# Optimization experiments

Hardware: AMD Instinct MI355X
Metric: run time of the kernel (lower is better)

Reference implementation:

```python
import math
import jax, jax.numpy as jnp
import numpy as np

NUM_HEADS, RAD_PTS, LVL_PTS = 8, 4, 1
P = RAD_PTS * LVL_PTS


def setup_inputs() -> dict:
    B, Nq, Din = 2, 21760, 256
    hw = np.array([[128, 128], [64, 64], [32, 32], [16, 16]], np.int64)
    sizes = hw[:, 0] * hw[:, 1]
    offs = np.concatenate([[0], np.cumsum(sizes)[:-1]]).astype(np.int64)
    Ns = int(sizes.sum())
    map_ids = np.tile(np.repeat(np.arange(4), sizes)[None], (B, 1)).astype(np.int64)

    key = jax.random.key(0)
    ks = jax.random.split(key, 8)
    in_feats = jax.random.normal(ks[0], (B, Nq, Din), jnp.float32)
    sample_feats = jax.random.normal(ks[1], (B, Ns, Din), jnp.float32)
    sample_priors = jax.random.uniform(ks[2], (B, Nq, 2), jnp.float32)

    # sample_offsets bias: radial grid init as in the torch module
    thetas = np.arange(NUM_HEADS) * (2.0 * math.pi / NUM_HEADS)
    grid = np.stack([np.cos(thetas), np.sin(thetas), np.zeros(NUM_HEADS)], 1)
    grid = grid / np.abs(grid).max(1, keepdims=True)
    grid = np.tile(grid.reshape(NUM_HEADS, 1, 1, 3), (1, RAD_PTS, LVL_PTS, 1))
    grid = grid * np.arange(1, RAD_PTS + 1).reshape(1, RAD_PTS, 1, 1)
    bo = jnp.asarray(grid.reshape(-1), jnp.float32)

    Wo = jax.random.normal(ks[3], (NUM_HEADS * P * 3, Din), jnp.float32) * 0.01
    Wa = jax.random.normal(ks[4], (NUM_HEADS * P, Din), jnp.float32) * 0.01
    ba = jnp.zeros((NUM_HEADS * P,), jnp.float32)
    s = 1.0 / np.sqrt(Din)
    Wv = jax.random.normal(ks[5], (Din, Din), jnp.float32) * s
    bv = jnp.zeros((Din,), jnp.float32)
    Wout = jax.random.normal(ks[6], (Din, Din), jnp.float32) * s
    bout = jnp.zeros((Din,), jnp.float32)

    return dict(in_feats=in_feats, sample_priors=sample_priors, sample_feats=sample_feats,
                map_hw=jnp.asarray(hw), map_offs=jnp.asarray(offs), map_ids=jnp.asarray(map_ids),
                Wo=Wo, bo=bo, Wa=Wa, ba=ba, Wv=Wv, bv=bv, Wout=Wout, bout=bout)


def _trilinear_sample(val, map_hw, map_offs, xy, z, L):
    # val [B,Ns,H,D]; xy [B,Q,H,P,2] normalized; z [B,Q,H,P] in ~[0,1]
    B, Ns, H, D = val.shape
    Q = xy.shape[1]
    val_t = val.transpose(0, 2, 1, 3)  # [B,H,Ns,D]
    x, y = xy[..., 0], xy[..., 1]
    lvl_f = z * (L - 1)
    l0 = jnp.floor(lvl_f).astype(jnp.int32)
    wz = lvl_f - l0.astype(lvl_f.dtype)

    def gather(idx):  # idx [B,Q,H,P] int32 -> [B,Q,H,P,D]
        it = idx.transpose(0, 2, 1, 3).reshape(B, H, Q * P, 1)
        g = jnp.take_along_axis(val_t, it, axis=2)  # [B,H,Q*P,D]
        return g.reshape(B, H, Q, P, D).transpose(0, 2, 1, 3, 4)

    def sample_level(lvl):  # bilinear sample within pyramid level `lvl` (zero padding)
        valid_l = (lvl >= 0) & (lvl < L)
        lc = jnp.clip(lvl, 0, L - 1)
        Hl = map_hw[lc, 0].astype(jnp.int32)
        Wl = map_hw[lc, 1].astype(jnp.int32)
        off = map_offs[lc].astype(jnp.int32)
        xf = x * Wl.astype(x.dtype) - 0.5
        yf = y * Hl.astype(x.dtype) - 0.5
        x0 = jnp.floor(xf).astype(jnp.int32)
        y0 = jnp.floor(yf).astype(jnp.int32)
        dx = xf - x0.astype(x.dtype)
        dy = yf - y0.astype(x.dtype)
        out = jnp.zeros((B, Q, H, P, D), x.dtype)
        corners = [(x0, y0, (1 - dx) * (1 - dy)), (x0 + 1, y0, dx * (1 - dy)),
                   (x0, y0 + 1, (1 - dx) * dy), (x0 + 1, y0 + 1, dx * dy)]
        for xi, yi, w in corners:
            ok = valid_l & (xi >= 0) & (xi < Wl) & (yi >= 0) & (yi < Hl)
            idx = off + jnp.clip(yi, 0, Hl - 1) * Wl + jnp.clip(xi, 0, Wl - 1)
            out = out + gather(idx) * (w * ok.astype(x.dtype))[..., None]
        return out

    return sample_level(l0) * (1 - wz)[..., None] + sample_level(l0 + 1) * wz[..., None]


def reference(in_feats, sample_priors, sample_feats, map_hw, map_offs, map_ids,
              Wo, bo, Wa, ba, Wv, bv, Wout, bout):
    B, Nq, _ = in_feats.shape
    Ns = sample_feats.shape[1]
    L = map_hw.shape[0]
    D = Wv.shape[0] // NUM_HEADS

    val = (sample_feats @ Wv.T + bv).reshape(B, Ns, NUM_HEADS, D)
    offs = (in_feats @ Wo.T + bo).reshape(B, Nq, NUM_HEADS, P, 3)

    # sample_priors last dim == 2: normalize offsets by (W, H) of the query's map
    norm = map_hw[:, ::-1][map_ids].astype(offs.dtype)  # [B,Nq,2] (w,h)
    sample_xy = sample_priors[:, :, None, None, :2] + offs[..., :2] / norm[:, :, None, None, :]

    lvl_off = jnp.arange(LVL_PTS, dtype=offs.dtype) - 0.5 * (LVL_PTS - 1)
    z_grid = map_ids[:, :, None, None, None].astype(offs.dtype) + lvl_off  # [B,Nq,1,1,Lp]
    z_grid = jnp.broadcast_to(z_grid, (B, Nq, NUM_HEADS, RAD_PTS, LVL_PTS)).reshape(B, Nq, NUM_HEADS, P)
    sample_z = (z_grid + jnp.tanh(offs[..., 2])) / (L - 1)

    attn = jax.nn.softmax((in_feats @ Wa.T + ba).reshape(B, Nq, NUM_HEADS, P), axis=3)

    sampled = _trilinear_sample(val, map_hw, map_offs, sample_xy, sample_z, L)  # [B,Nq,H,P,D]
    attn_feats = jnp.einsum('bqhpd,bqhp->bqhd', sampled, attn).reshape(B, Nq, NUM_HEADS * D)
    return attn_feats @ Wout.T + bout
```

## Files before the change

### kernel.cpp

```cpp
#include <hip/hip_runtime.h>
#include <hip/hip_bf16.h>
#include <math.h>

typedef __bf16 bf16x8 __attribute__((ext_vector_type(8)));
typedef float f32x4 __attribute__((ext_vector_type(4)));
typedef float f32x2 __attribute__((ext_vector_type(2)));
typedef unsigned short ushort8 __attribute__((ext_vector_type(8)));

static __device__ __forceinline__ unsigned short f2bf(float f) {
    union { float f; unsigned u; } c; c.f = f;
    unsigned r = c.u + 0x7FFFu + ((c.u >> 16) & 1u);
    return (unsigned short)(r >> 16);
}

static __device__ __forceinline__ void gload_lds16(
    const unsigned short* g, unsigned short* l)
{
    __builtin_amdgcn_global_load_lds(
        (const __attribute__((address_space(1))) void*)g,
        (__attribute__((address_space(3))) void*)l, 16, 0, 0);
}

__global__ __launch_bounds__(256) void convert_weights_hist(
    const float* __restrict__ Wv, const float* __restrict__ Wo,
    const float* __restrict__ Wa, const float* __restrict__ Wout,
    const float* __restrict__ bo, const float* __restrict__ ba,
    unsigned short* __restrict__ Wv_b, unsigned short* __restrict__ Woa_b,
    unsigned short* __restrict__ Wout_b, float* __restrict__ boa,
    const float* __restrict__ priors, int* __restrict__ counts,
    int BQ, int Nq)
{
    __shared__ int cnt[16];
    if (threadIdx.x < 16) cnt[threadIdx.x] = 0;
    __syncthreads();

    int gid = blockIdx.x * blockDim.x + threadIdx.x;
    int stride = gridDim.x * blockDim.x;
    for (int i = gid; i < 163840; i += stride) {
        if (i < 65536)       Wv_b[i] = f2bf(Wv[i]);
        else if (i < 90112)  Woa_b[i - 65536] = f2bf(Wo[i - 65536]);
        else if (i < 98304)  Woa_b[i - 65536] = f2bf(Wa[i - 90112]);
        else                 Wout_b[i - 98304] = f2bf(Wout[i - 98304]);
    }
    if (gid < 96)       boa[gid] = bo[gid];
    else if (gid < 128) boa[gid] = ba[gid - 96];

    for (int q = gid; q < BQ; q += stride) {
        int b = q / Nq;
        float py = priors[(size_t)q * 2 + 1];
        int band = min(7, max(0, (int)(py * 8.0f)));
        atomicAdd(&cnt[b * 8 + band], 1);
    }
    __syncthreads();
    if (threadIdx.x < 16 && cnt[threadIdx.x] > 0)
        atomicAdd(&counts[threadIdx.x], cnt[threadIdx.x]);
}

__global__ __launch_bounds__(256) void bucket_scatter(
    const float* __restrict__ priors, const int* __restrict__ counts,
    int* __restrict__ cursors, int* __restrict__ qidx, int BQ, int Nq)
{
    __shared__ int lcnt[16];
    __shared__ int lbase[16];
    const int tid = threadIdx.x;
    if (tid < 16) lcnt[tid] = 0;
    __syncthreads();
    int q = blockIdx.x * 256 + tid;
    int mybucket = 0, myslot = 0;
    bool valid = q < BQ;
    if (valid) {
        int b = q / Nq;
        float py = priors[(size_t)q * 2 + 1];
        int band = min(7, max(0, (int)(py * 8.0f)));
        mybucket = b * 8 + band;
        myslot = atomicAdd(&lcnt[mybucket], 1);
    }
    __syncthreads();
    if (tid < 16) {
        int base = 0;
        #pragma unroll
        for (int i = 0; i < 16; ++i) base += (i < tid) ? counts[i] : 0;
        lbase[tid] = base + atomicAdd(&cursors[tid], lcnt[tid]);
    }
    __syncthreads();
    if (valid) qidx[lbase[mybucket] + myslot] = q;
}

template<int WN, bool A_BF16, int OUT_MODE>
__global__ __launch_bounds__(WN * 64) void gemm_mfma(
    const void* __restrict__ Av, const unsigned short* __restrict__ W,
    const float* __restrict__ bias, void* __restrict__ Cv,
    int M, int N, int K, int NsPB)
{
    constexpr int BM = 64;
    constexpr int BN = WN * 64;
    constexpr int BK = 64;
    constexpr int NTHR = WN * 64;
    constexpr int LDP = 72;
    constexpr int ASZ = A_BF16 ? (BM * 64) : (BM * LDP);

    __shared__ __align__(16) unsigned short As[ASZ];
    __shared__ __align__(16) unsigned short Bs[BN * 64];

    const int bm  = blockIdx.x * BM;
    const int bn  = blockIdx.y * BN;
    const int tid = threadIdx.x;
    const int wid = tid >> 6;
    const int lane = tid & 63;
    const int lr = lane & 15;
    const int lg = lane >> 4;
    const int lrow = lane >> 3;
    const int lc16 = (lane & 7) ^ (lrow & 7);

    f32x4 acc[4][4];
    #pragma unroll
    for (int mi = 0; mi < 4; ++mi)
        #pragma unroll
        for (int ni = 0; ni < 4; ++ni)
            acc[mi][ni] = (f32x4){0.f, 0.f, 0.f, 0.f};

    for (int kt = 0; kt < K; kt += BK) {
        #pragma unroll
        for (int c = wid; c < BN / 8; c += WN) {
            const unsigned short* g =
                W + (size_t)(bn + c * 8 + lrow) * K + kt + lc16 * 8;
            gload_lds16(g, Bs + c * 512);
        }
        if (A_BF16) {
            const unsigned short* A = (const unsigned short*)Av;
            #pragma unroll
            for (int c = wid; c < BM / 8; c += WN) {
                const unsigned short* g =
                    A + (size_t)(bm + c * 8 + lrow) * K + kt + lc16 * 8;
                gload_lds16(g, As + c * 512);
            }
        } else {
            const float* A = (const float*)Av;
            #pragma unroll
            for (int u = tid; u < BM * 8; u += NTHR) {
                int r = u >> 3, kb = u & 7;
                const float* src = A + (size_t)(bm + r) * K + kt + kb * 8;
                float4 f0 = *(const float4*)(src);
                float4 f1 = *(const float4*)(src + 4);
                ushort8 v;
                v[0] = f2bf(f0.x); v[1] = f2bf(f0.y);
                v[2] = f2bf(f0.z); v[3] = f2bf(f0.w);
                v[4] = f2bf(f1.x); v[5] = f2bf(f1.y);
                v[6] = f2bf(f1.z); v[7] = f2bf(f1.w);
                *(ushort8*)(As + r * LDP + kb * 8) = v;
            }
        }
        __syncthreads();

        #pragma unroll
        for (int kk = 0; kk < 2; ++kk) {
            bf16x8 fa[4], fb[4];
            #pragma unroll
            for (int mi = 0; mi < 4; ++mi) {
                if (A_BF16) {
                    int row = mi * 16 + lr;
                    fa[mi] = *(const bf16x8*)(As + row * 64 +
                                              ((kk * 4 + lg) ^ (lr & 7)) * 8);
                } else {
                    fa[mi] = *(const bf16x8*)(As + (mi * 16 + lr) * LDP +
                                              kk * 32 + lg * 8);
                }
            }
            #pragma unroll
            for (int ni = 0; ni < 4; ++ni) {
                int row = wid * 64 + ni * 16 + lr;
                fb[ni] = *(const bf16x8*)(Bs + row * 64 +
                                          ((kk * 4 + lg) ^ (lr & 7)) * 8);
            }
            #pragma unroll
            for (int mi = 0; mi < 4; ++mi)
                #pragma unroll
                for (int ni = 0; ni < 4; ++ni)
                    acc[mi][ni] = __builtin_amdgcn_mfma_f32_16x16x32_bf16(
                        fa[mi], fb[ni], acc[mi][ni], 0, 0, 0);
        }
        __syncthreads();
    }

    if (OUT_MODE == 2) {
        const int b = bm / NsPB;
        const int ns_base = bm - b * NsPB;
        #pragma unroll
        for (int ni = 0; ni < 4; ++ni) {
            int col = wid * 64 + ni * 16 + lr;
            int h   = col >> 5;
            int ch  = col & 31;
            float bv = bias[col];
            unsigned short* dst = (unsigned short*)Cv +
                (size_t)(b * 8 + h) * NsPB * 32 + ch;
            #pragma unroll
            for (int mi = 0; mi < 4; ++mi) {
                #pragma unroll
                for (int r = 0; r < 4; ++r) {
                    int ns = ns_base + mi * 16 + lg * 4 + r;
                    dst[(size_t)ns * 32] = f2bf(acc[mi][ni][r] + bv);
                }
            }
        }
    } else {
        #pragma unroll
        for (int ni = 0; ni < 4; ++ni) {
            int col = bn + wid * 64 + ni * 16 + lr;
            float bv = bias[col];
            #pragma unroll
            for (int mi = 0; mi < 4; ++mi) {
                #pragma unroll
                for (int r = 0; r < 4; ++r) {
                    int row = bm + mi * 16 + lg * 4 + r;
                    if (OUT_MODE == 1) {
                        ((unsigned short*)Cv)[(size_t)row * N + col] =
                            f2bf(acc[mi][ni][r] + bv);
                    } else {
                        ((float*)Cv)[(size_t)row * N + col] = acc[mi][ni][r] + bv;
                    }
                }
            }
        }
    }
}

__global__ __launch_bounds__(256) void msda_sample_kernel(
    const float* __restrict__ C1,
    const float* __restrict__ priors,
    const unsigned short* __restrict__ val,
    const int*   __restrict__ map_hw,
    const int*   __restrict__ map_offs,
    const int*   __restrict__ map_ids,
    const int*   __restrict__ qidx,
    unsigned short* __restrict__ out,
    int Nq, int Ns)
{
    const int swz = (blockIdx.x & 7) * (gridDim.x >> 3) + (blockIdx.x >> 3);
    const int qh  = threadIdx.x >> 7;
    const int bq  = qidx[swz * 2 + qh];
    const int t   = threadIdx.x & 127;
    const int b   = bq / Nq;
    const int q   = bq - b * Nq;

    __shared__ float s_w[2][32][9];
    __shared__ int   s_i[2][32][9];
    __shared__ float s_red[2][32][9];

    if (t < 64) {
        const int hp = t >> 1;
        const int sl = t & 1;
        const float* sc = C1 + (size_t)bq * 128;
        float o0 = sc[hp * 3 + 0];
        float o1 = sc[hp * 3 + 1];
        float o2 = sc[hp * 3 + 2];
        float logit = sc[96 + hp];

        float m = logit;
        m = fmaxf(m, __shfl_xor(m, 2));
        m = fmaxf(m, __shfl_xor(m, 4));
        float e = expf(logit - m);
        float s = e;
        s += __shfl_xor(s, 2);
        s += __shfl_xor(s, 4);
        float attnw = e / s;

        int lid = map_ids[(size_t)b * Ns + q];
        float px = priors[(size_t)bq * 2 + 0];
        float py = priors[(size_t)bq * 2 + 1];
        int Hq = map_hw[lid * 2 + 0];
        int Wq = map_hw[lid * 2 + 1];
        float x = px + o0 / (float)Wq;
        float y = py + o1 / (float)Hq;

        float lvl_f = (float)lid + tanhf(o2);
        float l0f = floorf(lvl_f);
        int   l0  = (int)l0f;
        float wz  = lvl_f - l0f;

        const int   lv = l0 + sl;
        const float wl = sl ? wz : (1.0f - wz);
        float w4[4];
        int   i4[4];
        if (lv >= 0 && lv < 4) {
            int Hs  = map_hw[lv * 2 + 0];
            int Ws  = map_hw[lv * 2 + 1];
            int off = map_offs[lv];
            float xf = x * (float)Ws - 0.5f;
            float yf = y * (float)Hs - 0.5f;
            float x0f = floorf(xf), y0f = floorf(yf);
            int   x0  = (int)x0f,  y0  = (int)y0f;
            float dx = xf - x0f, dy = yf - y0f;
            #pragma unroll
            for (int j = 0; j < 4; ++j) {
                int xi = x0 + (j & 1);
                int yi = y0 + (j >> 1);
                float w = ((j & 1) ? dx : 1.0f - dx) *
                          ((j >> 1) ? dy : 1.0f - dy);
                bool ok = (xi >= 0) && (xi < Ws) && (yi >= 0) && (yi < Hs);
                w4[j] = ok ? (w * wl * attnw) : 0.0f;
                i4[j] = ok ? ((off + yi * Ws + xi) << 6) : 0;
            }
        } else {
            #pragma unroll
            for (int j = 0; j < 4; ++j) { w4[j] = 0.0f; i4[j] = 0; }
        }
        #pragma unroll
        for (int j = 0; j < 4; ++j) {
            s_w[qh][hp][sl * 4 + j] = w4[j];
            s_i[qh][hp][sl * 4 + j] = i4[j];
        }
    }
    __syncthreads();

    const int p  = t >> 5;
    const int s  = t & 31;
    const int h  = s >> 2;
    const int d8 = s & 3;
    const int hp = h * 4 + p;

    float w[8];
    int   ix[8];
    #pragma unroll
    for (int j = 0; j < 8; ++j) { w[j] = s_w[qh][hp][j]; ix[j] = s_i[qh][hp][j]; }

    const char* vbase = (const char*)(val + (size_t)(b * 8 + h) * Ns * 32) + d8 * 16;
    f32x2 acc2[4];
    #pragma unroll
    for (int k = 0; k < 4; ++k) acc2[k] = (f32x2){0.f, 0.f};

    #pragma unroll
    for (int j = 0; j < 8; ++j) {
        uint4 u = *(const uint4*)(vbase + ix[j]);
        f32x2 w2 = {w[j], w[j]};
        unsigned ua[4] = {u.x, u.y, u.z, u.w};
        #pragma unroll
        for (int k = 0; k < 4; ++k) {
            union { unsigned u; float f; } lo, hi;
            lo.u = ua[k] << 16;
            hi.u = ua[k] & 0xffff0000u;
            f32x2 v2 = {lo.f, hi.f};
            acc2[k] += w2 * v2;
        }
    }

    #pragma unroll
    for (int k = 0; k < 4; ++k) {
        acc2[k][0] += __shfl_xor(acc2[k][0], 32);
        acc2[k][1] += __shfl_xor(acc2[k][1], 32);
    }

    if (t >= 64 && t < 96) {
        #pragma unroll
        for (int k = 0; k < 4; ++k) {
            s_red[qh][t - 64][2 * k]     = acc2[k][0];
            s_red[qh][t - 64][2 * k + 1] = acc2[k][1];
        }
    }
    __syncthreads();

    if (t < 32) {
        ushort8 o;
        #pragma unroll
        for (int k = 0; k < 4; ++k) {
            o[2 * k]     = f2bf(acc2[k][0] + s_red[qh][t][2 * k]);
            o[2 * k + 1] = f2bf(acc2[k][1] + s_red[qh][t][2 * k + 1]);
        }
        *(ushort8*)(out + (size_t)bq * 256 + t * 8) = o;
    }
}

extern "C" void kernel_launch(void* const* d_in, const int* in_sizes, int n_in,
                              void* d_out, int out_size, void* d_ws, size_t ws_size,
                              hipStream_t stream) {
    const float* in_feats      = (const float*)d_in[0];
    const float* sample_priors = (const float*)d_in[1];
    const float* sample_feats  = (const float*)d_in[2];
    const int*   map_hw        = (const int*)d_in[3];
    const int*   map_offs      = (const int*)d_in[4];
    const int*   map_ids       = (const int*)d_in[5];
    const float* Wo            = (const float*)d_in[6];
    const float* bo            = (const float*)d_in[7];
    const float* Wa            = (const float*)d_in[8];
    const float* ba            = (const float*)d_in[9];
    const float* Wv            = (const float*)d_in[10];
    const float* bv            = (const float*)d_in[11];
    const float* Wout          = (const float*)d_in[12];
    const float* bout          = (const float*)d_in[13];
    float* out = (float*)d_out;

    const int B = 2, Nq = 21760, Din = 256;
    const int Ns = in_sizes[2] / (B * Din);
    const int BQ = B * Nq;

    unsigned short* val = (unsigned short*)d_out;
    float* C1 = (float*)d_ws;
    unsigned short* af = (unsigned short*)((char*)d_ws + (size_t)BQ * 128 * 4);
    char* wbase = (char*)d_ws + (size_t)BQ * 128 * 4 + (size_t)BQ * 256 * 2;
    unsigned short* Wv_b   = (unsigned short*)wbase;
    unsigned short* Woa_b  = Wv_b + 65536;
    unsigned short* Wout_b = Woa_b + 32768;
    float* boa = (float*)(Wout_b + 65536);
    int* bws  = (int*)(boa + 128);
    int* qidx = bws + 32;

    hipMemsetAsync(bws, 0, 128, stream);

    convert_weights_hist<<<dim3(160), dim3(256), 0, stream>>>(
        Wv, Wo, Wa, Wout, bo, ba, Wv_b, Woa_b, Wout_b, boa,
        sample_priors, bws, BQ, Nq);

    bucket_scatter<<<dim3((BQ + 255) / 256), dim3(256), 0, stream>>>(
        sample_priors, bws, bws + 16, qidx, BQ, Nq);

    gemm_mfma<4, false, 2><<<dim3(BQ / 64, 1), dim3(256), 0, stream>>>(
        sample_feats, Wv_b, bv, val, B * Ns, 256, Din, Ns);

    gemm_mfma<2, false, 0><<<dim3(BQ / 64, 1), dim3(128), 0, stream>>>(
        in_feats, Woa_b, boa, C1, BQ, 128, Din, Ns);

    msda_sample_kernel<<<dim3(BQ / 2), dim3(256), 0, stream>>>(
        C1, sample_priors, val, map_hw, map_offs, map_ids, qidx, af, Nq, Ns);

    gemm_mfma<4, true, 0><<<dim3(BQ / 64, 1), dim3(256), 0, stream>>>(
        af, Wout_b, bout, out, BQ, 256, Din, Ns);
}
```

Measured before the change: 114.2 us.

## Process one query per block with adjacent-x threads and shuffle-only reduction

The sampling kernel now handles one query per 256-thread block instead of two, with the grid doubled. Each thread covers one x-corner of one bilinear row for a 64-byte slice, so neighbouring threads load adjacent memory. Per-row records (row base, packed x/width, two weights) are written to shared memory, and the cross-point reduction uses warp shuffles instead of a second shared-memory pass and barrier. This trades twice as many blocks and a single-query workload per block for fewer barriers and more coalesced gathers.

```diff
diff --git a/kernel.cpp b/kernel.cpp
--- a/kernel.cpp
+++ b/kernel.cpp
@@ -236,15 +236,12 @@
     int Nq, int Ns)
 {
     const int swz = (blockIdx.x & 7) * (gridDim.x >> 3) + (blockIdx.x >> 3);
-    const int qh  = threadIdx.x >> 7;
-    const int bq  = qidx[swz * 2 + qh];
-    const int t   = threadIdx.x & 127;
+    const int bq  = qidx[swz];
+    const int t   = threadIdx.x;
     const int b   = bq / Nq;
     const int q   = bq - b * Nq;
 
-    __shared__ float s_w[2][32][9];
-    __shared__ int   s_i[2][32][9];
-    __shared__ float s_red[2][32][9];
+    __shared__ __align__(16) float s_row[32 * 20];
 
     if (t < 64) {
         const int hp = t >> 1;
@@ -278,9 +275,12 @@
         float wz  = lvl_f - l0f;
 
         const int   lv = l0 + sl;
-        const float wl = sl ? wz : (1.0f - wz);
-        float w4[4];
-        int   i4[4];
+        const float wl = (sl ? wz : (1.0f - wz)) * attnw;
+
+        float w0[2] = {0.f, 0.f}, w1[2] = {0.f, 0.f};
+        int   rb[2] = {0, 0};
+        int   xw[2];
+        xw[0] = xw[1] = (1 << 16) | 512;
         if (lv >= 0 && lv < 4) {
             int Hs  = map_hw[lv * 2 + 0];
             int Ws  = map_hw[lv * 2 + 1];
@@ -290,48 +290,55 @@
             float x0f = floorf(xf), y0f = floorf(yf);
             int   x0  = (int)x0f,  y0  = (int)y0f;
             float dx = xf - x0f, dy = yf - y0f;
-            #pragma unroll
-            for (int j = 0; j < 4; ++j) {
-                int xi = x0 + (j & 1);
-                int yi = y0 + (j >> 1);
-                float w = ((j & 1) ? dx : 1.0f - dx) *
-                          ((j >> 1) ? dy : 1.0f - dy);
-                bool ok = (xi >= 0) && (xi < Ws) && (yi >= 0) && (yi < Hs);
-                w4[j] = ok ? (w * wl * attnw) : 0.0f;
-                i4[j] = ok ? ((off + yi * Ws + xi) << 6) : 0;
-            }
-        } else {
-            #pragma unroll
-            for (int j = 0; j < 4; ++j) { w4[j] = 0.0f; i4[j] = 0; }
-        }
-        #pragma unroll
-        for (int j = 0; j < 4; ++j) {
-            s_w[qh][hp][sl * 4 + j] = w4[j];
-            s_i[qh][hp][sl * 4 + j] = i4[j];
-        }
-    }
-    __syncthreads();
-
-    const int p  = t >> 5;
-    const int s  = t & 31;
-    const int h  = s >> 2;
-    const int d8 = s & 3;
-    const int hp = h * 4 + p;
-
-    float w[8];
-    int   ix[8];
-    #pragma unroll
-    for (int j = 0; j < 8; ++j) { w[j] = s_w[qh][hp][j]; ix[j] = s_i[qh][hp][j]; }
-
-    const char* vbase = (const char*)(val + (size_t)(b * 8 + h) * Ns * 32) + d8 * 16;
+            int   xp = (Ws << 16) | ((x0 + 512) & 0xffff);
+            #pragma unroll
+            for (int yc = 0; yc < 2; ++yc) {
+                int  yi = y0 + yc;
+                bool vy = (yi >= 0) && (yi < Hs);
+                int  yic = min(max(yi, 0), Hs - 1);
+                float wy = (yc ? dy : (1.0f - dy)) * wl * (vy ? 1.0f : 0.0f);
+                rb[yc] = off + yic * Ws;
+                xw[yc] = xp;
+                w0[yc] = wy * (1.0f - dx);
+                w1[yc] = wy * dx;
+            }
+        }
+        #pragma unroll
+        for (int yc = 0; yc < 2; ++yc) {
+            int j = sl * 2 + yc;
+            f32x4 rec;
+            rec[0] = __int_as_float(rb[yc]);
+            rec[1] = __int_as_float(xw[yc]);
+            rec[2] = w0[yc];
+            rec[3] = w1[yc];
+            *(f32x4*)(s_row + hp * 20 + j * 4) = rec;
+        }
+    }
+    __syncthreads();
+
+    const int hp   = t >> 3;
+    const int d16  = t & 7;
+    const int xg   = (t >> 2) & 1;
+    const int boff = (t & 3) * 16;
+
+    const char* vbase = (const char*)(val + (size_t)(b * 8 + (hp >> 2)) * Ns * 32);
     f32x2 acc2[4];
     #pragma unroll
     for (int k = 0; k < 4; ++k) acc2[k] = (f32x2){0.f, 0.f};
 
     #pragma unroll
-    for (int j = 0; j < 8; ++j) {
-        uint4 u = *(const uint4*)(vbase + ix[j]);
-        f32x2 w2 = {w[j], w[j]};
+    for (int j = 0; j < 4; ++j) {
+        f32x4 rec = *(const f32x4*)(s_row + hp * 20 + j * 4);
+        int   rb = __float_as_int(rec[0]);
+        int   xw = __float_as_int(rec[1]);
+        float w  = xg ? rec[3] : rec[2];
+        int   Ws = xw >> 16;
+        int   xi = (xw & 0xffff) - 512 + xg;
+        bool  in = (xi >= 0) && (xi < Ws);
+        int   xic = min(max(xi, 0), Ws - 1);
+        w = in ? w : 0.0f;
+        uint4 u = *(const uint4*)(vbase + (size_t)(unsigned)((rb + xic) << 6) + boff);
+        f32x2 w2 = {w, w};
         unsigned ua[4] = {u.x, u.y, u.z, u.w};
         #pragma unroll
         for (int k = 0; k < 4; ++k) {
@@ -345,27 +352,24 @@
 
     #pragma unroll
     for (int k = 0; k < 4; ++k) {
-        acc2[k][0] += __shfl_xor(acc2[k][0], 32);
-        acc2[k][1] += __shfl_xor(acc2[k][1], 32);
-    }
-
-    if (t >= 64 && t < 96) {
+        acc2[k][0] += __shfl_xor(acc2[k][0], 4);
+        acc2[k][1] += __shfl_xor(acc2[k][1], 4);
+        acc2[k][0] += __shfl_xor(acc2[k][0], 8);
+        acc2[k][1] += __shfl_xor(acc2[k][1], 8);
+        acc2[k][0] += __shfl_xor(acc2[k][0], 16);
+        acc2[k][1] += __shfl_xor(acc2[k][1], 16);
+    }
+
+    if ((t & 28) == 0) {
+        const int h  = t >> 5;
+        const int d8 = t & 3;
+        ushort8 o;
         #pragma unroll
         for (int k = 0; k < 4; ++k) {
-            s_red[qh][t - 64][2 * k]     = acc2[k][0];
-            s_red[qh][t - 64][2 * k + 1] = acc2[k][1];
-        }
-    }
-    __syncthreads();
-
-    if (t < 32) {
-        ushort8 o;
-        #pragma unroll
-        for (int k = 0; k < 4; ++k) {
-            o[2 * k]     = f2bf(acc2[k][0] + s_red[qh][t][2 * k]);
-            o[2 * k + 1] = f2bf(acc2[k][1] + s_red[qh][t][2 * k + 1]);
-        }
-        *(ushort8*)(out + (size_t)bq * 256 + t * 8) = o;
+            o[2 * k]     = f2bf(acc2[k][0]);
+            o[2 * k + 1] = f2bf(acc2[k][1]);
+        }
+        *(ushort8*)(out + (size_t)bq * 256 + h * 32 + d8 * 8) = o;
     }
 }
 
@@ -418,7 +422,7 @@
     gemm_mfma<2, false, 0><<<dim3(BQ / 64, 1), dim3(128), 0, stream>>>(
         in_feats, Woa_b, boa, C1, BQ, 128, Din, Ns);
 
-    msda_sample_kernel<<<dim3(BQ / 2), dim3(256), 0, stream>>>(
+    msda_sample_kernel<<<dim3(BQ), dim3(256), 0, stream>>>(
         C1, sample_priors, val, map_hw, map_offs, map_ids, qidx, af, Nq, Ns);
 
     gemm_mfma<4, true, 0><<<dim3(BQ / 64, 1), dim3(256), 0, stream>>>(
```

New measurement: 142.9 us. 25.2% more time.

## Map one query per wavefront in sampling kernel, removing block barriers

Applied to the files above, without the earlier changes.

Restructures the sampling kernel so each 64-lane wavefront handles a whole query, with four queries per block instead of two. Sample weights and indices now go through wave-private LDS with only an lgkmcnt wait in place of __syncthreads. The final reduction across points becomes a lane-pair shuffle rather than a shared-memory exchange. Each lane now issues 16 gathers instead of 8, which means fewer threads in flight per query and more registers per lane. The wavefront-synchronous LDS pattern also relies on lanes within a wave executing in lockstep.

```diff
diff --git a/kernel.cpp b/kernel.cpp
--- a/kernel.cpp
+++ b/kernel.cpp
@@ -235,20 +235,18 @@
     unsigned short* __restrict__ out,
     int Nq, int Ns)
 {
-    const int swz = (blockIdx.x & 7) * (gridDim.x >> 3) + (blockIdx.x >> 3);
-    const int qh  = threadIdx.x >> 7;
-    const int bq  = qidx[swz * 2 + qh];
-    const int t   = threadIdx.x & 127;
-    const int b   = bq / Nq;
-    const int q   = bq - b * Nq;
-
-    __shared__ float s_w[2][32][9];
-    __shared__ int   s_i[2][32][9];
-    __shared__ float s_red[2][32][9];
-
-    if (t < 64) {
-        const int hp = t >> 1;
-        const int sl = t & 1;
+    const int swz  = (blockIdx.x & 7) * (gridDim.x >> 3) + (blockIdx.x >> 3);
+    const int wvi  = threadIdx.x >> 6;
+    const int lane = threadIdx.x & 63;
+    const int bq   = qidx[swz * 4 + wvi];
+    const int b    = bq / Nq;
+    const int q    = bq - b * Nq;
+
+    __shared__ __align__(16) float s_rec[4][4][128];
+
+    {
+        const int hp = lane >> 1;
+        const int sl = lane & 1;
         const float* sc = C1 + (size_t)bq * 128;
         float o0 = sc[hp * 3 + 0];
         float o1 = sc[hp * 3 + 1];
@@ -304,68 +302,70 @@
             #pragma unroll
             for (int j = 0; j < 4; ++j) { w4[j] = 0.0f; i4[j] = 0; }
         }
-        #pragma unroll
-        for (int j = 0; j < 4; ++j) {
-            s_w[qh][hp][sl * 4 + j] = w4[j];
-            s_i[qh][hp][sl * 4 + j] = i4[j];
-        }
-    }
-    __syncthreads();
-
-    const int p  = t >> 5;
-    const int s  = t & 31;
-    const int h  = s >> 2;
-    const int d8 = s & 3;
-    const int hp = h * 4 + p;
-
-    float w[8];
-    int   ix[8];
-    #pragma unroll
-    for (int j = 0; j < 8; ++j) { w[j] = s_w[qh][hp][j]; ix[j] = s_i[qh][hp][j]; }
-
-    const char* vbase = (const char*)(val + (size_t)(b * 8 + h) * Ns * 32) + d8 * 16;
+        f32x4 wrec = {w4[0], w4[1], w4[2], w4[3]};
+        f32x4 irec = {__int_as_float(i4[0]), __int_as_float(i4[1]),
+                      __int_as_float(i4[2]), __int_as_float(i4[3])};
+        *(f32x4*)&s_rec[wvi][sl][hp * 4]     = wrec;
+        *(f32x4*)&s_rec[wvi][2 + sl][hp * 4] = irec;
+    }
+    asm volatile("s_waitcnt lgkmcnt(0)" ::: "memory");
+
+    const int p2 = lane & 1;
+    const int d8 = (lane >> 1) & 3;
+    const int h  = lane >> 3;
+    const char* vbase = (const char*)(val + (size_t)(b * 8 + h) * Ns * 32)
+                        + d8 * 16;
+
     f32x2 acc2[4];
     #pragma unroll
     for (int k = 0; k < 4; ++k) acc2[k] = (f32x2){0.f, 0.f};
 
     #pragma unroll
-    for (int j = 0; j < 8; ++j) {
-        uint4 u = *(const uint4*)(vbase + ix[j]);
-        f32x2 w2 = {w[j], w[j]};
-        unsigned ua[4] = {u.x, u.y, u.z, u.w};
-        #pragma unroll
-        for (int k = 0; k < 4; ++k) {
-            union { unsigned u; float f; } lo, hi;
-            lo.u = ua[k] << 16;
-            hi.u = ua[k] & 0xffff0000u;
-            f32x2 v2 = {lo.f, hi.f};
-            acc2[k] += w2 * v2;
+    for (int pp = 0; pp < 2; ++pp) {
+        const int hp = h * 4 + p2 + pp * 2;
+        f32x4 wlo = *(const f32x4*)&s_rec[wvi][0][hp * 4];
+        f32x4 whi = *(const f32x4*)&s_rec[wvi][1][hp * 4];
+        f32x4 xlo = *(const f32x4*)&s_rec[wvi][2][hp * 4];
+        f32x4 xhi = *(const f32x4*)&s_rec[wvi][3][hp * 4];
+
+        uint4 u[8];
+        #pragma unroll
+        for (int j = 0; j < 4; ++j)
+            u[j] = *(const uint4*)(vbase + __float_as_int(xlo[j]));
+        #pragma unroll
+        for (int j = 0; j < 4; ++j)
+            u[4 + j] = *(const uint4*)(vbase + __float_as_int(xhi[j]));
+
+        #pragma unroll
+        for (int j = 0; j < 8; ++j) {
+            float w = (j < 4) ? wlo[j] : whi[j - 4];
+            f32x2 w2 = {w, w};
+            unsigned ua[4] = {u[j].x, u[j].y, u[j].z, u[j].w};
+            #pragma unroll
+            for (int k = 0; k < 4; ++k) {
+                union { unsigned u; float f; } lo, hi;
+                lo.u = ua[k] << 16;
+                hi.u = ua[k] & 0xffff0000u;
+                f32x2 v2 = {lo.f, hi.f};
+                acc2[k] += w2 * v2;
+            }
         }
     }
 
     #pragma unroll
     for (int k = 0; k < 4; ++k) {
-        acc2[k][0] += __shfl_xor(acc2[k][0], 32);
-        acc2[k][1] += __shfl_xor(acc2[k][1], 32);
-    }
-
-    if (t >= 64 && t < 96) {
+        acc2[k][0] += __shfl_xor(acc2[k][0], 1);
+        acc2[k][1] += __shfl_xor(acc2[k][1], 1);
+    }
+
+    if (p2 == 0) {
+        ushort8 o;
         #pragma unroll
         for (int k = 0; k < 4; ++k) {
-            s_red[qh][t - 64][2 * k]     = acc2[k][0];
-            s_red[qh][t - 64][2 * k + 1] = acc2[k][1];
-        }
-    }
-    __syncthreads();
-
-    if (t < 32) {
-        ushort8 o;
-        #pragma unroll
-        for (int k = 0; k < 4; ++k) {
-            o[2 * k]     = f2bf(acc2[k][0] + s_red[qh][t][2 * k]);
-            o[2 * k + 1] = f2bf(acc2[k][1] + s_red[qh][t][2 * k + 1]);
-        }
-        *(ushort8*)(out + (size_t)bq * 256 + t * 8) = o;
+            o[2 * k]     = f2bf(acc2[k][0]);
+            o[2 * k + 1] = f2bf(acc2[k][1]);
+        }
+        *(ushort8*)(out + (size_t)bq * 256 + h * 32 + d8 * 8) = o;
     }
 }
 
@@ -418,7 +418,7 @@
     gemm_mfma<2, false, 0><<<dim3(BQ / 64, 1), dim3(128), 0, stream>>>(
         in_feats, Woa_b, boa, C1, BQ, 128, Din, Ns);
 
-    msda_sample_kernel<<<dim3(BQ / 2), dim3(256), 0, stream>>>(
+    msda_sample_kernel<<<dim3(BQ / 4), dim3(256), 0, stream>>>(
         C1, sample_priors, val, map_hw, map_offs, map_ids, qidx, af, Nq, Ns);
 
     gemm_mfma<4, true, 0><<<dim3(BQ / 64, 1), dim3(256), 0, stream>>>(
```

After: 108.4 us. -5.1%, faster.
